# Optimization experiments

Hardware: AMD Instinct MI355X
Metric: run time of the kernel (lower is better)

## Reference

```python
import jax, jax.numpy as jnp
import numpy as np

N_NODES = 50000


def _sage_conv(x, src, dst, Wl, Wr, bl, num_nodes):
    # PyG SAGEConv (mean aggr): out = lin_l(mean_{j in N(i)} x_j) + lin_r(x_i)
    # messages flow src -> dst
    agg = jax.ops.segment_sum(x[src], dst, num_segments=num_nodes)          # [N, F]
    deg = jax.ops.segment_sum(jnp.ones_like(dst, dtype=x.dtype), dst,
                              num_segments=num_nodes)                       # [N]
    agg = agg / jnp.maximum(deg, 1.0)[:, None]
    return agg @ Wl + bl + x @ Wr


def setup_inputs() -> dict:
    key = jax.random.key(0)
    ks = jax.random.split(key, 9)
    F_in, H, C, E = 256, 256, 40, 800000
    s = lambda fan: 1.0 / np.sqrt(fan)
    x = jax.random.normal(ks[0], (N_NODES, F_in), dtype=jnp.float32)
    edge_index = jax.random.randint(ks[1], (2, E), 0, N_NODES, dtype=jnp.int32)
    W1l = jax.random.normal(ks[2], (F_in, H), dtype=jnp.float32) * s(F_in)
    W1r = jax.random.normal(ks[3], (F_in, H), dtype=jnp.float32) * s(F_in)
    b1 = jnp.zeros((H,), dtype=jnp.float32)
    W2l = jax.random.normal(ks[4], (H, C), dtype=jnp.float32) * s(H)
    W2r = jax.random.normal(ks[5], (H, C), dtype=jnp.float32) * s(H)
    b2 = jnp.zeros((C,), dtype=jnp.float32)
    Q = jax.random.normal(ks[6], (E // 2, C), dtype=jnp.float32) * s(E // 2)
    return {"x": x, "edge_index": edge_index, "W1l": W1l, "b1": b1,
            "W1r": W1r, "W2l": W2l, "b2": b2, "W2r": W2r, "Q": Q}


def reference(x, edge_index, W1l, b1, W1r, W2l, b2, W2r, Q):
    # Eval mode: F.dropout with training=False is identity.
    src, dst = edge_index[0], edge_index[1]
    h = _sage_conv(x, src, dst, W1l, W1r, b1, N_NODES)
    h = jax.nn.elu(h)
    out = _sage_conv(h, src, dst, W2l, W2r, b2, N_NODES)
    return (out, Q)
```

## Files before the change

kernel.cpp:

```cpp
#include <hip/hip_runtime.h>
#include <hip/hip_bf16.h>
#include <cstddef>

#define N_NODES 50000
#define M_PAD 50048
#define BSTRIDE 64

typedef __attribute__((ext_vector_type(8))) short short8;
typedef __attribute__((ext_vector_type(4))) float floatx4;

__device__ inline unsigned short f2bf(float f) {
    union { float f; unsigned u; } v; v.f = f;
    unsigned r = v.u + 0x7fff + ((v.u >> 16) & 1);
    return (unsigned short)(r >> 16);
}
__device__ inline float bfbits_lo(unsigned u) {
    union { unsigned u; float f; } v; v.u = u << 16; return v.f;
}
__device__ inline float bfbits_hi(unsigned u) {
    union { unsigned u; float f; } v; v.u = u & 0xffff0000u; return v.f;
}

__device__ inline void gload16(const void* g, void* l) {
    __builtin_amdgcn_global_load_lds(
        (const __attribute__((address_space(1))) unsigned int*)g,
        (__attribute__((address_space(3))) unsigned int*)l, 16, 0, 0);
}

#define PREP_NT (2048 * 256)
__global__ __launch_bounds__(256) void prep_count(
    const float* __restrict__ x,
    const float* __restrict__ W1l, const float* __restrict__ W1r,
    const float* __restrict__ W2l, const float* __restrict__ W2r,
    unsigned short* __restrict__ Abuf, unsigned short* __restrict__ B1t,
    unsigned short* __restrict__ B2t,
    const int* __restrict__ src, const int* __restrict__ dst,
    int* __restrict__ deg, unsigned short* __restrict__ bucket, int E) {
    int gtid = blockIdx.x * 256 + threadIdx.x;

    int e0 = gtid, e1 = gtid + PREP_NT;
    bool h0 = e0 < E, h1 = e1 < E;
    int d0 = 0, d1 = 0, s0 = 0, s1 = 0, r0 = 0, r1 = 0;
    if (h0) { d0 = dst[e0]; s0 = src[e0]; r0 = atomicAdd(&deg[d0], 1); }
    if (h1) { d1 = dst[e1]; s1 = src[e1]; r1 = atomicAdd(&deg[d1], 1); }

    for (int i = gtid; i < N_NODES * 32; i += PREP_NT) {
        int row = i >> 5;
        int c8 = i & 31;
        const float4* xp = reinterpret_cast<const float4*>(x + (size_t)row * 256 + c8 * 8);
        float4 v0 = xp[0], v1 = xp[1];
        uint4 o;
        o.x = (unsigned)f2bf(v0.x) | ((unsigned)f2bf(v0.y) << 16);
        o.y = (unsigned)f2bf(v0.z) | ((unsigned)f2bf(v0.w) << 16);
        o.z = (unsigned)f2bf(v1.x) | ((unsigned)f2bf(v1.y) << 16);
        o.w = (unsigned)f2bf(v1.z) | ((unsigned)f2bf(v1.w) << 16);
        *reinterpret_cast<uint4*>(Abuf + (size_t)row * 512 + 256 + c8 * 8) = o;
    }
    if (gtid < 256 * 512) {
        int n = gtid >> 9, k = gtid & 511;
        float v = (k < 256) ? W1l[(size_t)k * 256 + n] : W1r[(size_t)(k - 256) * 256 + n];
        B1t[(size_t)n * 512 + k] = f2bf(v);
    }
    if (gtid < 80 * 256) {
        int n = gtid >> 8, k = gtid & 255;
        float v = (n < 40) ? W2l[(size_t)k * 40 + n] : W2r[(size_t)k * 40 + (n - 40)];
        B2t[(size_t)n * 256 + k] = f2bf(v);
    }

    if (h0) bucket[(size_t)d0 * BSTRIDE + r0] = (unsigned short)s0;
    if (h1) bucket[(size_t)d1 * BSTRIDE + r1] = (unsigned short)s1;
}

__global__ __launch_bounds__(256) void aggregate1(
    const unsigned short* __restrict__ Abuf, const int* __restrict__ deg,
    const unsigned short* __restrict__ bucket,
    unsigned short* __restrict__ AbufOut, int N) {
    int node = blockIdx.x * 4 + (threadIdx.x >> 6);
    if (node >= N) return;
    int lane = threadIdx.x & 63;
    int half = lane >> 5;
    int dlane = lane & 31;
    const unsigned short* base = Abuf + 256 + (size_t)dlane * 8;
    const unsigned short* bkt = bucket + (size_t)node * BSTRIDE;
    int dg = deg[node];
    float a0 = 0.f, a1 = 0.f, a2 = 0.f, a3 = 0.f;
    float a4 = 0.f, a5 = 0.f, a6 = 0.f, a7 = 0.f;
    int k = half;
    for (; k + 15 < dg; k += 16) {
        uint4 v[8];
        #pragma unroll
        for (int u = 0; u < 8; ++u) {
            int j = bkt[k + u * 2];
            v[u] = *reinterpret_cast<const uint4*>(base + (size_t)j * 512);
        }
        #pragma unroll
        for (int u = 0; u < 8; ++u) {
            a0 += bfbits_lo(v[u].x); a1 += bfbits_hi(v[u].x);
            a2 += bfbits_lo(v[u].y); a3 += bfbits_hi(v[u].y);
            a4 += bfbits_lo(v[u].z); a5 += bfbits_hi(v[u].z);
            a6 += bfbits_lo(v[u].w); a7 += bfbits_hi(v[u].w);
        }
    }
    for (; k + 7 < dg; k += 8) {
        uint4 v[4];
        #pragma unroll
        for (int u = 0; u < 4; ++u) {
            int j = bkt[k + u * 2];
            v[u] = *reinterpret_cast<const uint4*>(base + (size_t)j * 512);
        }
        #pragma unroll
        for (int u = 0; u < 4; ++u) {
            a0 += bfbits_lo(v[u].x); a1 += bfbits_hi(v[u].x);
            a2 += bfbits_lo(v[u].y); a3 += bfbits_hi(v[u].y);
            a4 += bfbits_lo(v[u].z); a5 += bfbits_hi(v[u].z);
            a6 += bfbits_lo(v[u].w); a7 += bfbits_hi(v[u].w);
        }
    }
    for (; k < dg; k += 2) {
        int j = bkt[k];
        uint4 v = *reinterpret_cast<const uint4*>(base + (size_t)j * 512);
        a0 += bfbits_lo(v.x); a1 += bfbits_hi(v.x); a2 += bfbits_lo(v.y); a3 += bfbits_hi(v.y);
        a4 += bfbits_lo(v.z); a5 += bfbits_hi(v.z); a6 += bfbits_lo(v.w); a7 += bfbits_hi(v.w);
    }
    a0 += __shfl_xor(a0, 32, 64); a1 += __shfl_xor(a1, 32, 64);
    a2 += __shfl_xor(a2, 32, 64); a3 += __shfl_xor(a3, 32, 64);
    a4 += __shfl_xor(a4, 32, 64); a5 += __shfl_xor(a5, 32, 64);
    a6 += __shfl_xor(a6, 32, 64); a7 += __shfl_xor(a7, 32, 64);
    if (half == 0) {
        float s = 1.0f / (float)(dg > 1 ? dg : 1);
        uint4 w;
        w.x = (unsigned)f2bf(a0 * s) | ((unsigned)f2bf(a1 * s) << 16);
        w.y = (unsigned)f2bf(a2 * s) | ((unsigned)f2bf(a3 * s) << 16);
        w.z = (unsigned)f2bf(a4 * s) | ((unsigned)f2bf(a5 * s) << 16);
        w.w = (unsigned)f2bf(a6 * s) | ((unsigned)f2bf(a7 * s) << 16);
        *reinterpret_cast<uint4*>(AbufOut + (size_t)node * 512 + dlane * 8) = w;
    }
}

__global__ __launch_bounds__(256) void gemm1_mfma(
    const unsigned short* __restrict__ Abuf,
    const unsigned short* __restrict__ B1t,
    const float* __restrict__ bias,
    unsigned short* __restrict__ H,
    int M) {
    __shared__ unsigned short As[2][64 * 64];
    __shared__ unsigned short Bs[2][128 * 64];
    int tid = threadIdx.x;
    int row0 = blockIdx.y * 64;
    int bn = blockIdx.x;
    int wid = tid >> 6, lane = tid & 63;
    int wm = (wid >> 1) * 32;
    int wn = (wid & 1) * 64;
    int fr = lane & 15, fq = lane >> 4;

    int lrow8 = lane >> 3;
    int gco = ((lane & 7) ^ lrow8) * 8;
    const unsigned short* gA0 = Abuf + (size_t)(row0 + wid * 16 + 0 + lrow8) * 512 + gco;
    const unsigned short* gA1 = Abuf + (size_t)(row0 + wid * 16 + 8 + lrow8) * 512 + gco;
    const unsigned short* gB0 = B1t + (size_t)(bn * 128 + wid * 32 + 0  + lrow8) * 512 + gco;
    const unsigned short* gB1 = B1t + (size_t)(bn * 128 + wid * 32 + 8  + lrow8) * 512 + gco;
    const unsigned short* gB2 = B1t + (size_t)(bn * 128 + wid * 32 + 16 + lrow8) * 512 + gco;
    const unsigned short* gB3 = B1t + (size_t)(bn * 128 + wid * 32 + 24 + lrow8) * 512 + gco;

    floatx4 acc[2][4] = {};

    #define STAGE(buf, k0)                                       \
        gload16(gA0 + (k0), &As[buf][(wid * 16 + 0) * 64]);      \
        gload16(gA1 + (k0), &As[buf][(wid * 16 + 8) * 64]);      \
        gload16(gB0 + (k0), &Bs[buf][(wid * 32 + 0) * 64]);      \
        gload16(gB1 + (k0), &Bs[buf][(wid * 32 + 8) * 64]);      \
        gload16(gB2 + (k0), &Bs[buf][(wid * 32 + 16) * 64]);     \
        gload16(gB3 + (k0), &Bs[buf][(wid * 32 + 24) * 64]);

    #define COMPUTE(buf)                                                                  \
        {                                                                                 \
            _Pragma("unroll")                                                             \
            for (int kc = 0; kc < 2; ++kc) {                                              \
                short8 af[2], bfr[4];                                                     \
                _Pragma("unroll")                                                         \
                for (int mi = 0; mi < 2; ++mi) {                                          \
                    int row = wm + mi * 16 + fr;                                          \
                    af[mi] = *reinterpret_cast<const short8*>(                            \
                        &As[buf][row * 64 + (((kc * 4 + fq) ^ (fr & 7)) * 8)]);           \
                }                                                                         \
                _Pragma("unroll")                                                         \
                for (int ni = 0; ni < 4; ++ni) {                                          \
                    int row = wn + ni * 16 + fr;                                          \
                    bfr[ni] = *reinterpret_cast<const short8*>(                           \
                        &Bs[buf][row * 64 + (((kc * 4 + fq) ^ (fr & 7)) * 8)]);           \
                }                                                                         \
                _Pragma("unroll")                                                         \
                for (int mi = 0; mi < 2; ++mi)                                            \
                    _Pragma("unroll")                                                     \
                    for (int ni = 0; ni < 4; ++ni)                                        \
                        acc[mi][ni] = __builtin_amdgcn_mfma_f32_16x16x32_bf16(            \
                            af[mi], bfr[ni], acc[mi][ni], 0, 0, 0);                       \
            }                                                                             \
        }

    STAGE(0, 0);
    STAGE(1, 64);
    asm volatile("s_waitcnt vmcnt(6)" ::: "memory");
    __builtin_amdgcn_s_barrier();
    __builtin_amdgcn_sched_barrier(0);
    int cur = 0;
    #pragma unroll 1
    for (int t = 0; t < 6; ++t) {
        COMPUTE(cur);
        __builtin_amdgcn_sched_barrier(0);
        __builtin_amdgcn_s_barrier();
        STAGE(cur, (t + 2) * 64);
        asm volatile("s_waitcnt vmcnt(6)" ::: "memory");
        __builtin_amdgcn_s_barrier();
        __builtin_amdgcn_sched_barrier(0);
        cur ^= 1;
    }
    COMPUTE(cur);
    __builtin_amdgcn_sched_barrier(0);
    asm volatile("s_waitcnt vmcnt(0)" ::: "memory");
    __builtin_amdgcn_s_barrier();
    __builtin_amdgcn_sched_barrier(0);
    COMPUTE(cur ^ 1);
    #undef STAGE
    #undef COMPUTE

    #pragma unroll
    for (int ni = 0; ni < 4; ++ni) {
        int gcol = bn * 128 + wn + ni * 16 + fr;
        float bb = bias[gcol];
        #pragma unroll
        for (int mi = 0; mi < 2; ++mi) {
            #pragma unroll
            for (int r = 0; r < 4; ++r) {
                int grow = row0 + wm + mi * 16 + fq * 4 + r;
                float t = acc[mi][ni][r] + bb;
                t = (t > 0.f) ? t : expm1f(t);
                H[(size_t)grow * 256 + gcol] = f2bf(t);
            }
        }
    }
}

__global__ __launch_bounds__(256) void gemm2_mfma(
    const unsigned short* __restrict__ Hb,
    const unsigned short* __restrict__ B2t,
    const float* __restrict__ b2,
    unsigned short* __restrict__ Plb,
    float* __restrict__ Pr,
    int M) {
    __shared__ unsigned short Bsm[80 * 256];
    __shared__ unsigned short As[2][64 * 64];
    int tid = threadIdx.x;
    int row0 = blockIdx.x * 64;
    int wid = tid >> 6, lane = tid & 63;
    int wm = wid * 16;
    int fr = lane & 15, fq = lane >> 4;

    for (int c = tid; c < 2560; c += 256) {
        int n = c >> 5, ci = c & 31;
        short8 v = *reinterpret_cast<const short8*>(B2t + (size_t)n * 256 + ci * 8);
        *reinterpret_cast<short8*>(&Bsm[n * 256 + ((ci ^ (n & 7)) * 8)]) = v;
    }

    int lrow8 = lane >> 3;
    int gco = ((lane & 7) ^ lrow8) * 8;
    const unsigned short* gA0 = Hb + (size_t)(row0 + wid * 16 + 0 + lrow8) * 256 + gco;
    const unsigned short* gA1 = Hb + (size_t)(row0 + wid * 16 + 8 + lrow8) * 256 + gco;

    floatx4 acc[5] = {};

    #define STAGE2(buf, k0)                                      \
        gload16(gA0 + (k0), &As[buf][(wid * 16 + 0) * 64]);      \
        gload16(gA1 + (k0), &As[buf][(wid * 16 + 8) * 64]);

    #define COMPUTE2(buf, k0)                                                             \
        {                                                                                 \
            _Pragma("unroll")                                                             \
            for (int kc = 0; kc < 2; ++kc) {                                              \
                short8 af;                                                                \
                {                                                                         \
                    int row = wm + fr;                                                    \
                    af = *reinterpret_cast<const short8*>(                                \
                        &As[buf][row * 64 + (((kc * 4 + fq) ^ (fr & 7)) * 8)]);           \
                }                                                                         \
                _Pragma("unroll")                                                         \
                for (int ni = 0; ni < 5; ++ni) {                                          \
                    int n = ni * 16 + fr;                                                 \
                    int c = ((k0) >> 3) + kc * 4 + fq;                                    \
                    short8 bfr = *reinterpret_cast<const short8*>(                        \
                        &Bsm[n * 256 + ((c ^ (n & 7)) * 8)]);                             \
                    acc[ni] = __builtin_amdgcn_mfma_f32_16x16x32_bf16(                    \
                        af, bfr, acc[ni], 0, 0, 0);                                       \
                }                                                                         \
            }                                                                             \
        }

    STAGE2(0, 0);
    __syncthreads();
    int cur = 0;
    #pragma unroll 1
    for (int t = 0; t < 3; ++t) {
        STAGE2(cur ^ 1, (t + 1) * 64);
        COMPUTE2(cur, t * 64);
        __syncthreads();
        cur ^= 1;
    }
    COMPUTE2(cur, 192);
    #undef STAGE2
    #undef COMPUTE2

    #pragma unroll
    for (int r = 0; r < 4; ++r) {
        int grow = row0 + wm + fq * 4 + r;
        if (grow < M) {
            #pragma unroll
            for (int ni = 0; ni < 5; ++ni) {
                int col = ni * 16 + fr;
                float v = acc[ni][r];
                if (col < 40)
                    Plb[(size_t)grow * 40 + col] = f2bf(v);
                else
                    Pr[(size_t)grow * 40 + (col - 40)] = v + b2[col - 40];
            }
        }
    }
}

__global__ __launch_bounds__(256) void final_kernel(
    const unsigned short* __restrict__ Plb, const float* __restrict__ Pr,
    const int* __restrict__ deg, const unsigned short* __restrict__ bucket,
    float* __restrict__ out, int N) {
    int wv = blockIdx.x * 4 + (threadIdx.x >> 6);
    int lid = threadIdx.x & 63;
    int sub = lid / 20;
    if (sub >= 3) return;
    int node = wv * 3 + sub;
    if (node >= N) return;
    int lane = lid - sub * 20;
    const unsigned short* bkt = bucket + (size_t)node * BSTRIDE;
    int dg = deg[node];
    float s0 = 0.f, s1 = 0.f;
    int k = 0;
    for (; k + 4 <= dg; k += 4) {
        unsigned v0 = *reinterpret_cast<const unsigned*>(Plb + (size_t)bkt[k]     * 40 + lane * 2);
        unsigned v1 = *reinterpret_cast<const unsigned*>(Plb + (size_t)bkt[k + 1] * 40 + lane * 2);
        unsigned v2 = *reinterpret_cast<const unsigned*>(Plb + (size_t)bkt[k + 2] * 40 + lane * 2);
        unsigned v3 = *reinterpret_cast<const unsigned*>(Plb + (size_t)bkt[k + 3] * 40 + lane * 2);
        s0 += bfbits_lo(v0) + bfbits_lo(v1) + bfbits_lo(v2) + bfbits_lo(v3);
        s1 += bfbits_hi(v0) + bfbits_hi(v1) + bfbits_hi(v2) + bfbits_hi(v3);
    }
    for (; k < dg; ++k) {
        unsigned v = *reinterpret_cast<const unsigned*>(Plb + (size_t)bkt[k] * 40 + lane * 2);
        s0 += bfbits_lo(v);
        s1 += bfbits_hi(v);
    }
    float inv = 1.0f / (float)(dg > 1 ? dg : 1);
    float2 pr = *reinterpret_cast<const float2*>(Pr + (size_t)node * 40 + lane * 2);
    float2 o;
    o.x = s0 * inv + pr.x;
    o.y = s1 * inv + pr.y;
    *reinterpret_cast<float2*>(out + (size_t)node * 40 + lane * 2) = o;
}


extern "C" void kernel_launch(void* const* d_in, const int* in_sizes, int n_in,
                              void* d_out, int out_size, void* d_ws, size_t ws_size,
                              hipStream_t stream) {
    const float* x   = (const float*)d_in[0];
    const int*   ei  = (const int*)d_in[1];
    const float* W1l = (const float*)d_in[2];
    const float* b1  = (const float*)d_in[3];
    const float* W1r = (const float*)d_in[4];
    const float* W2l = (const float*)d_in[5];
    const float* b2  = (const float*)d_in[6];
    const float* W2r = (const float*)d_in[7];
    const float* Q   = (const float*)d_in[8];
    const int E = in_sizes[1] / 2;
    const int N = N_NODES;
    const int* src = ei;
    const int* dst = ei + E;

    unsigned short* Abuf = (unsigned short*)d_ws;
    unsigned short* h    = Abuf + (size_t)M_PAD * 512;
    unsigned short* B1t  = h + (size_t)M_PAD * 256;
    unsigned short* B2t  = B1t + 256 * 512;
    unsigned short* Plb  = B2t + 80 * 256;
    float* Pr      = (float*)(Plb + (size_t)N * 40 + 32);
    int*   deg     = (int*)(Pr + (size_t)N * 40);
    unsigned short* bucket = (unsigned short*)(deg + N);

    float* out = (float*)d_out;

    hipMemsetAsync(deg, 0, sizeof(int) * (size_t)N, stream);
    prep_count<<<2048, 256, 0, stream>>>(x, W1l, W1r, W2l, W2r,
                                         Abuf, B1t, B2t, src, dst, deg, bucket, E);

    aggregate1<<<(N + 3) / 4, 256, 0, stream>>>(Abuf, deg, bucket, Abuf, N);

    gemm1_mfma<<<dim3(2, M_PAD / 64), 256, 0, stream>>>(Abuf, B1t, b1, h, N);
    gemm2_mfma<<<M_PAD / 64, 256, 0, stream>>>(h, B2t, b2, Plb, Pr, N);
    final_kernel<<<(N + 11) / 12, 256, 0, stream>>>(Plb, Pr, deg, bucket, out, N);

    hipMemcpyAsync(out + (size_t)N * 40, Q, sizeof(float) * (size_t)in_sizes[8],
                   hipMemcpyDeviceToDevice, stream);
}
```

Before: 213.8 us.

## Load GEMM1 B operand directly into registers instead of staging through LDS

The weight tile B is now read from global memory straight into MFMA-ready register fragments, with register double-buffering, and is no longer copied asynchronously into shared memory. The A tile still uses the LDS double buffer, but the pipeline switches from explicit vmcnt waits and sched_barriers to a simple __syncthreads-based prefetch loop. This cuts LDS usage and LDS reads for B, which may allow higher occupancy. In exchange it raises register pressure and makes each wave fetch its own B fragments, with no sharing across waves. It also relies on the compiler's own wait insertion, which can serialize the global_load_lds traffic.

```diff
diff --git a/kernel.cpp b/kernel.cpp
--- a/kernel.cpp
+++ b/kernel.cpp
@@ -144,7 +144,6 @@
     unsigned short* __restrict__ H,
     int M) {
     __shared__ unsigned short As[2][64 * 64];
-    __shared__ unsigned short Bs[2][128 * 64];
     int tid = threadIdx.x;
     int row0 = blockIdx.y * 64;
     int bn = blockIdx.x;
@@ -157,26 +156,35 @@
     int gco = ((lane & 7) ^ lrow8) * 8;
     const unsigned short* gA0 = Abuf + (size_t)(row0 + wid * 16 + 0 + lrow8) * 512 + gco;
     const unsigned short* gA1 = Abuf + (size_t)(row0 + wid * 16 + 8 + lrow8) * 512 + gco;
-    const unsigned short* gB0 = B1t + (size_t)(bn * 128 + wid * 32 + 0  + lrow8) * 512 + gco;
-    const unsigned short* gB1 = B1t + (size_t)(bn * 128 + wid * 32 + 8  + lrow8) * 512 + gco;
-    const unsigned short* gB2 = B1t + (size_t)(bn * 128 + wid * 32 + 16 + lrow8) * 512 + gco;
-    const unsigned short* gB3 = B1t + (size_t)(bn * 128 + wid * 32 + 24 + lrow8) * 512 + gco;
+
+    const unsigned short* gBrow0 = B1t + (size_t)(bn * 128 + wn +  0 + fr) * 512 + fq * 8;
+    const unsigned short* gBrow1 = B1t + (size_t)(bn * 128 + wn + 16 + fr) * 512 + fq * 8;
+    const unsigned short* gBrow2 = B1t + (size_t)(bn * 128 + wn + 32 + fr) * 512 + fq * 8;
+    const unsigned short* gBrow3 = B1t + (size_t)(bn * 128 + wn + 48 + fr) * 512 + fq * 8;
 
     floatx4 acc[2][4] = {};
-
-    #define STAGE(buf, k0)                                       \
-        gload16(gA0 + (k0), &As[buf][(wid * 16 + 0) * 64]);      \
-        gload16(gA1 + (k0), &As[buf][(wid * 16 + 8) * 64]);      \
-        gload16(gB0 + (k0), &Bs[buf][(wid * 32 + 0) * 64]);      \
-        gload16(gB1 + (k0), &Bs[buf][(wid * 32 + 8) * 64]);      \
-        gload16(gB2 + (k0), &Bs[buf][(wid * 32 + 16) * 64]);     \
-        gload16(gB3 + (k0), &Bs[buf][(wid * 32 + 24) * 64]);
-
-    #define COMPUTE(buf)                                                                  \
+    short8 bc[2][4], bnx[2][4];
+
+    #define STAGE_A(buf, k0)                                 \
+        gload16(gA0 + (k0), &As[buf][(wid * 16 + 0) * 64]);  \
+        gload16(gA1 + (k0), &As[buf][(wid * 16 + 8) * 64]);
+
+    #define LOADB(dst, k0)                                                               \
+        {                                                                                \
+            _Pragma("unroll")                                                            \
+            for (int kc = 0; kc < 2; ++kc) {                                             \
+                dst[kc][0] = *reinterpret_cast<const short8*>(gBrow0 + (k0) + kc * 32);  \
+                dst[kc][1] = *reinterpret_cast<const short8*>(gBrow1 + (k0) + kc * 32);  \
+                dst[kc][2] = *reinterpret_cast<const short8*>(gBrow2 + (k0) + kc * 32);  \
+                dst[kc][3] = *reinterpret_cast<const short8*>(gBrow3 + (k0) + kc * 32);  \
+            }                                                                            \
+        }
+
+    #define COMPUTE(buf, breg)                                                            \
         {                                                                                 \
             _Pragma("unroll")                                                             \
             for (int kc = 0; kc < 2; ++kc) {                                              \
-                short8 af[2], bfr[4];                                                     \
+                short8 af[2];                                                             \
                 _Pragma("unroll")                                                         \
                 for (int mi = 0; mi < 2; ++mi) {                                          \
                     int row = wm + mi * 16 + fr;                                          \
@@ -184,44 +192,34 @@
                         &As[buf][row * 64 + (((kc * 4 + fq) ^ (fr & 7)) * 8)]);           \
                 }                                                                         \
                 _Pragma("unroll")                                                         \
-                for (int ni = 0; ni < 4; ++ni) {                                          \
-                    int row = wn + ni * 16 + fr;                                          \
-                    bfr[ni] = *reinterpret_cast<const short8*>(                           \
-                        &Bs[buf][row * 64 + (((kc * 4 + fq) ^ (fr & 7)) * 8)]);           \
-                }                                                                         \
-                _Pragma("unroll")                                                         \
                 for (int mi = 0; mi < 2; ++mi)                                            \
                     _Pragma("unroll")                                                     \
                     for (int ni = 0; ni < 4; ++ni)                                        \
                         acc[mi][ni] = __builtin_amdgcn_mfma_f32_16x16x32_bf16(            \
-                            af[mi], bfr[ni], acc[mi][ni], 0, 0, 0);                       \
+                            af[mi], breg[kc][ni], acc[mi][ni], 0, 0, 0);                  \
             }                                                                             \
         }
 
-    STAGE(0, 0);
-    STAGE(1, 64);
-    asm volatile("s_waitcnt vmcnt(6)" ::: "memory");
-    __builtin_amdgcn_s_barrier();
-    __builtin_amdgcn_sched_barrier(0);
+    STAGE_A(0, 0);
+    LOADB(bc, 0);
+    __syncthreads();
     int cur = 0;
     #pragma unroll 1
-    for (int t = 0; t < 6; ++t) {
-        COMPUTE(cur);
-        __builtin_amdgcn_sched_barrier(0);
-        __builtin_amdgcn_s_barrier();
-        STAGE(cur, (t + 2) * 64);
-        asm volatile("s_waitcnt vmcnt(6)" ::: "memory");
-        __builtin_amdgcn_s_barrier();
-        __builtin_amdgcn_sched_barrier(0);
+    for (int t = 0; t < 7; ++t) {
+        STAGE_A(cur ^ 1, (t + 1) * 64);
+        LOADB(bnx, (t + 1) * 64);
+        COMPUTE(cur, bc);
+        __syncthreads();
+        #pragma unroll
+        for (int kc = 0; kc < 2; ++kc)
+            #pragma unroll
+            for (int ni = 0; ni < 4; ++ni)
+                bc[kc][ni] = bnx[kc][ni];
         cur ^= 1;
     }
-    COMPUTE(cur);
-    __builtin_amdgcn_sched_barrier(0);
-    asm volatile("s_waitcnt vmcnt(0)" ::: "memory");
-    __builtin_amdgcn_s_barrier();
-    __builtin_amdgcn_sched_barrier(0);
-    COMPUTE(cur ^ 1);
-    #undef STAGE
+    COMPUTE(cur, bc);
+    #undef STAGE_A
+    #undef LOADB
     #undef COMPUTE
 
     #pragma unroll
```

After: 245.4 us. +14.8%, slower.
